# Kernel tuning notes

Hardware: AMD Instinct MI355X
Metric: run time of the kernel (lower is better)

The kernel has to match this reference:

```python
import jax, jax.numpy as jnp
import numpy as np


def setup_inputs() -> dict:
    key = jax.random.key(0)
    k1, k2, k3, k4 = jax.random.split(key, 4)
    B, L, H, E = 2, 10000, 8, 64
    NE = 160000
    return {
        "queries": jax.random.normal(k1, (B, L, H, E), dtype=jnp.float32),
        "keys": jax.random.normal(k2, (B, L, H, E), dtype=jnp.float32),
        "values": jax.random.normal(k3, (B, L, H, E), dtype=jnp.float32),
        "adj": jax.random.randint(k4, (2, NE), 0, L, dtype=jnp.int64),
    }


def reference(queries, keys, values, adj):
    # queries/keys/values: [B, L, H, E]; adj: [2, NE] (row 0 = dst group, row 1 = src)
    B, L, H, E = queries.shape
    softmax_temp = 1.0 / (E ** 0.5)
    dst = adj[0]
    src = adj[1]

    # edge-gather dot product: qk[b, e, h] = sum_d q[b, dst[e], h, d] * k[b, src[e], h, d]
    qk = jnp.sum(queries[:, dst] * keys[:, src], axis=-1) * softmax_temp  # [B, NE, H]

    # segment softmax grouped by destination node (dropout is identity at eval)
    qk_e = qk.transpose(1, 0, 2)  # [NE, B, H] (segment ops act on leading axis)
    seg_max = jax.ops.segment_max(qk_e, dst, num_segments=L)  # [L, B, H]
    ex = jnp.exp(qk_e - seg_max[dst])
    seg_sum = jax.ops.segment_sum(ex, dst, num_segments=L)  # [L, B, H]
    alpha = ex / (seg_sum[dst] + 1e-16)  # [NE, B, H]

    # spmm: gather v at src, weight by alpha, scatter-add to dst
    weighted = values[:, src] * alpha.transpose(1, 0, 2)[..., None]  # [B, NE, H, E]
    out = jnp.zeros_like(values).at[:, dst].add(weighted)  # [B, L, H, E]
    return out
```

## Files before the change

kernel.cpp:

```cpp
#include <hip/hip_runtime.h>

#define BB 2
#define HH 8
#define EE 64
#define ROW (HH * EE)
#define CHUNK 16

__device__ inline unsigned short f2bf(float f) {
  unsigned int u = __float_as_uint(f);
  u = (u + 0x7fffu + ((u >> 16) & 1u)) >> 16;
  return (unsigned short)u;
}

__global__ __launch_bounds__(256) void convert_kernel(
    const float* __restrict__ k, const float* __restrict__ v,
    unsigned short* __restrict__ kbf, unsigned short* __restrict__ vbf,
    int n4) {
  int i = blockIdx.x * blockDim.x + threadIdx.x;
  if (i >= n4) return;
  float4 kf = ((const float4*)k)[i];
  float4 vf = ((const float4*)v)[i];
  ushort4 ko = make_ushort4(f2bf(kf.x), f2bf(kf.y), f2bf(kf.z), f2bf(kf.w));
  ushort4 vo = make_ushort4(f2bf(vf.x), f2bf(vf.y), f2bf(vf.z), f2bf(vf.w));
  ((ushort4*)kbf)[i] = ko;
  ((ushort4*)vbf)[i] = vo;
}

__global__ __launch_bounds__(256) void hist_kernel(
    const int* __restrict__ dst, int* __restrict__ counts, int NE) {
  int e = blockIdx.x * blockDim.x + threadIdx.x;
  if (e >= NE) return;
  atomicAdd(&counts[dst[e]], 1);
}

__global__ __launch_bounds__(1024) void scan_kernel(
    const int* __restrict__ counts, int* __restrict__ offsets, int L) {
  __shared__ int sums[1024];
  int tid = threadIdx.x;
  int chunk = (L + 1023) / 1024;
  int beg = tid * chunk;
  int end = min(beg + chunk, L);
  int s = 0;
  for (int i = beg; i < end; ++i) s += counts[i];
  sums[tid] = s;
  __syncthreads();
  for (int off = 1; off < 1024; off <<= 1) {
    int val = 0;
    if (tid >= off) val = sums[tid - off];
    __syncthreads();
    if (tid >= off) sums[tid] += val;
    __syncthreads();
  }
  int run = (tid > 0) ? sums[tid - 1] : 0;
  for (int i = beg; i < end; ++i) {
    offsets[i] = run;
    run += counts[i];
  }
  if (tid == 1023) offsets[L] = run;
}

__global__ __launch_bounds__(256) void fill_csr_kernel(
    const int* __restrict__ dst, const int* __restrict__ src,
    const int* __restrict__ offsets, int* __restrict__ cursor,
    int* __restrict__ csr_src, int NE) {
  int e = blockIdx.x * blockDim.x + threadIdx.x;
  if (e >= NE) return;
  int d = dst[e];
  int pos = atomicAdd(&cursor[d], 1);
  csr_src[offsets[d] + pos] = src[e];
}

__device__ inline void bf8_unpack(uint4 u, float* f) {
  f[0] = __uint_as_float(u.x << 16);
  f[1] = __uint_as_float(u.x & 0xffff0000u);
  f[2] = __uint_as_float(u.y << 16);
  f[3] = __uint_as_float(u.y & 0xffff0000u);
  f[4] = __uint_as_float(u.z << 16);
  f[5] = __uint_as_float(u.z & 0xffff0000u);
  f[6] = __uint_as_float(u.w << 16);
  f[7] = __uint_as_float(u.w & 0xffff0000u);
}

__global__ __launch_bounds__(256) void fused_attn_kernel(
    const float* __restrict__ q, const unsigned short* __restrict__ kbf,
    const unsigned short* __restrict__ vbf, const int* __restrict__ offsets,
    const int* __restrict__ csr_src, float* __restrict__ out, int L) {
  int wid = blockIdx.x * (blockDim.x >> 6) + (threadIdx.x >> 6);
  int lane = threadIdx.x & 63;
  if (wid >= L * BB) return;
  int d = wid >> 1;
  int b = wid & 1;
  int beg = offsets[d];
  int end = offsets[d + 1];

  const float4* qrow = (const float4*)(q + ((size_t)b * L + d) * ROW);
  float4 q0 = qrow[lane * 2 + 0];
  float4 q1 = qrow[lane * 2 + 1];

  float m = -INFINITY;
  float l_run = 0.0f;
  float acc[8];
#pragma unroll
  for (int i = 0; i < 8; ++i) acc[i] = 0.0f;

  const uint4* kb_base = (const uint4*)(kbf + (size_t)b * L * ROW);
  const uint4* vb_base = (const uint4*)(vbf + (size_t)b * L * ROW);

  for (int t0 = beg; t0 < end; t0 += CHUNK) {
    int cnt = min(CHUNK, end - t0);
    float qk[CHUNK];
    int srcs[CHUNK];
    float cmax = -INFINITY;
#pragma unroll
    for (int i = 0; i < CHUNK; ++i) {
      qk[i] = -INFINITY;
      if (i < cnt) {
        int s = csr_src[t0 + i];
        srcs[i] = s;
        uint4 kk = kb_base[(size_t)s * (ROW / 8) + lane];
        float kf[8];
        bf8_unpack(kk, kf);
        float p = q0.x * kf[0] + q0.y * kf[1] + q0.z * kf[2] + q0.w * kf[3] +
                  q1.x * kf[4] + q1.y * kf[5] + q1.z * kf[6] + q1.w * kf[7];
        p += __shfl_xor(p, 1);
        p += __shfl_xor(p, 2);
        p += __shfl_xor(p, 4);
        p *= 0.125f;
        qk[i] = p;
        cmax = fmaxf(cmax, p);
      }
    }
    float mnew = fmaxf(m, cmax);
    float scale = __expf(m - mnew);
    l_run *= scale;
#pragma unroll
    for (int i = 0; i < 8; ++i) acc[i] *= scale;
    m = mnew;
#pragma unroll
    for (int i = 0; i < CHUNK; ++i) {
      if (i < cnt) {
        float a = __expf(qk[i] - m);
        l_run += a;
        uint4 vv = vb_base[(size_t)srcs[i] * (ROW / 8) + lane];
        float vf[8];
        bf8_unpack(vv, vf);
#pragma unroll
        for (int j = 0; j < 8; ++j) acc[j] += a * vf[j];
      }
    }
  }
  float r = 1.0f / (l_run + 1e-16f);
  float4* orow = (float4*)(out + ((size_t)b * L + d) * ROW);
  orow[lane * 2 + 0] = make_float4(acc[0] * r, acc[1] * r, acc[2] * r, acc[3] * r);
  orow[lane * 2 + 1] = make_float4(acc[4] * r, acc[5] * r, acc[6] * r, acc[7] * r);
}

extern "C" void kernel_launch(void* const* d_in, const int* in_sizes, int n_in,
                              void* d_out, int out_size, void* d_ws, size_t ws_size,
                              hipStream_t stream) {
  const float* q = (const float*)d_in[0];
  const float* k = (const float*)d_in[1];
  const float* v = (const float*)d_in[2];
  const int* adj = (const int*)d_in[3];

  const int NE = in_sizes[3] / 2;
  const int L = in_sizes[0] / (BB * HH * EE);
  const int* dst = adj;
  const int* src = adj + NE;
  const int nelem = BB * L * HH * EE;

  char* ws = (char*)d_ws;
  size_t off = 0;
  unsigned short* kbf = (unsigned short*)(ws + off); off += (size_t)nelem * 2;
  unsigned short* vbf = (unsigned short*)(ws + off); off += (size_t)nelem * 2;
  int* counts = (int*)(ws + off);   off += (size_t)L * 4;
  int* offsets = (int*)(ws + off);  off += (size_t)(L + 1) * 4;
  int* cursor = (int*)(ws + off);   off += (size_t)L * 4;
  int* csr_src = (int*)(ws + off);  off += (size_t)NE * 4;

  hipMemsetAsync(counts, 0, (size_t)L * 4, stream);
  hipMemsetAsync(cursor, 0, (size_t)L * 4, stream);

  int n4 = nelem / 4;
  convert_kernel<<<(n4 + 255) / 256, 256, 0, stream>>>(k, v, kbf, vbf, n4);

  hist_kernel<<<(NE + 255) / 256, 256, 0, stream>>>(dst, counts, NE);
  scan_kernel<<<1, 1024, 0, stream>>>(counts, offsets, L);
  fill_csr_kernel<<<(NE + 255) / 256, 256, 0, stream>>>(dst, src, offsets, cursor, csr_src, NE);

  int nwaves = L * BB;
  fused_attn_kernel<<<(nwaves + 3) / 4, 256, 0, stream>>>(
      q, kbf, vbf, offsets, csr_src, (float*)d_out, L);
}
```

Baseline: 287.8 us.

## Fuse convert with histogram, reuse counts as cursor, prefetch K/V per chunk

Folds the bf16 conversion and the destination histogram into one kernel. The scan now zeroes the counts array so fill_csr can reuse it as the cursor, which removes one memset, one buffer and one launch. In the attention kernel, all K and V rows for a chunk are loaded up front so the gather loads can be in flight together. CHUNK is halved to 8 to limit the extra register pressure from holding 16 uint4 values. The scan reads and writes counts through two __restrict__ pointers that alias the same array, but each thread reads an element before zeroing it, so it is likely safe.

```diff
diff --git a/kernel.cpp b/kernel.cpp
--- a/kernel.cpp
+++ b/kernel.cpp
@@ -4,7 +4,7 @@
 #define HH 8
 #define EE 64
 #define ROW (HH * EE)
-#define CHUNK 16
+#define CHUNK 8
 
 __device__ inline unsigned short f2bf(float f) {
   unsigned int u = __float_as_uint(f);
@@ -12,36 +12,33 @@
   return (unsigned short)u;
 }
 
-__global__ __launch_bounds__(256) void convert_kernel(
+__global__ __launch_bounds__(256) void convert_hist_kernel(
     const float* __restrict__ k, const float* __restrict__ v,
     unsigned short* __restrict__ kbf, unsigned short* __restrict__ vbf,
-    int n4) {
+    const int* __restrict__ dst, int* __restrict__ counts,
+    int n4, int NE) {
   int i = blockIdx.x * blockDim.x + threadIdx.x;
-  if (i >= n4) return;
-  float4 kf = ((const float4*)k)[i];
-  float4 vf = ((const float4*)v)[i];
-  ushort4 ko = make_ushort4(f2bf(kf.x), f2bf(kf.y), f2bf(kf.z), f2bf(kf.w));
-  ushort4 vo = make_ushort4(f2bf(vf.x), f2bf(vf.y), f2bf(vf.z), f2bf(vf.w));
-  ((ushort4*)kbf)[i] = ko;
-  ((ushort4*)vbf)[i] = vo;
-}
-
-__global__ __launch_bounds__(256) void hist_kernel(
-    const int* __restrict__ dst, int* __restrict__ counts, int NE) {
-  int e = blockIdx.x * blockDim.x + threadIdx.x;
-  if (e >= NE) return;
-  atomicAdd(&counts[dst[e]], 1);
+  if (i < n4) {
+    float4 kf = ((const float4*)k)[i];
+    float4 vf = ((const float4*)v)[i];
+    ((ushort4*)kbf)[i] = make_ushort4(f2bf(kf.x), f2bf(kf.y), f2bf(kf.z), f2bf(kf.w));
+    ((ushort4*)vbf)[i] = make_ushort4(f2bf(vf.x), f2bf(vf.y), f2bf(vf.z), f2bf(vf.w));
+  }
+  if (i < NE) {
+    atomicAdd(&counts[dst[i]], 1);
+  }
 }
 
 __global__ __launch_bounds__(1024) void scan_kernel(
-    const int* __restrict__ counts, int* __restrict__ offsets, int L) {
+    const int* __restrict__ counts_in, int* __restrict__ counts_mut,
+    int* __restrict__ offsets, int L) {
   __shared__ int sums[1024];
   int tid = threadIdx.x;
   int chunk = (L + 1023) / 1024;
   int beg = tid * chunk;
   int end = min(beg + chunk, L);
   int s = 0;
-  for (int i = beg; i < end; ++i) s += counts[i];
+  for (int i = beg; i < end; ++i) s += counts_in[i];
   sums[tid] = s;
   __syncthreads();
   for (int off = 1; off < 1024; off <<= 1) {
@@ -54,7 +51,8 @@
   int run = (tid > 0) ? sums[tid - 1] : 0;
   for (int i = beg; i < end; ++i) {
     offsets[i] = run;
-    run += counts[i];
+    run += counts_in[i];
+    counts_mut[i] = 0;
   }
   if (tid == 1023) offsets[L] = run;
 }
@@ -108,18 +106,23 @@
 
   for (int t0 = beg; t0 < end; t0 += CHUNK) {
     int cnt = min(CHUNK, end - t0);
+    uint4 kk[CHUNK], vv[CHUNK];
+#pragma unroll
+    for (int i = 0; i < CHUNK; ++i) {
+      if (i < cnt) {
+        int s = csr_src[t0 + i];
+        kk[i] = kb_base[(size_t)s * (ROW / 8) + lane];
+        vv[i] = vb_base[(size_t)s * (ROW / 8) + lane];
+      }
+    }
     float qk[CHUNK];
-    int srcs[CHUNK];
     float cmax = -INFINITY;
 #pragma unroll
     for (int i = 0; i < CHUNK; ++i) {
       qk[i] = -INFINITY;
       if (i < cnt) {
-        int s = csr_src[t0 + i];
-        srcs[i] = s;
-        uint4 kk = kb_base[(size_t)s * (ROW / 8) + lane];
         float kf[8];
-        bf8_unpack(kk, kf);
+        bf8_unpack(kk[i], kf);
         float p = q0.x * kf[0] + q0.y * kf[1] + q0.z * kf[2] + q0.w * kf[3] +
                   q1.x * kf[4] + q1.y * kf[5] + q1.z * kf[6] + q1.w * kf[7];
         p += __shfl_xor(p, 1);
@@ -141,9 +144,8 @@
       if (i < cnt) {
         float a = __expf(qk[i] - m);
         l_run += a;
-        uint4 vv = vb_base[(size_t)srcs[i] * (ROW / 8) + lane];
         float vf[8];
-        bf8_unpack(vv, vf);
+        bf8_unpack(vv[i], vf);
 #pragma unroll
         for (int j = 0; j < 8; ++j) acc[j] += a * vf[j];
       }
@@ -175,18 +177,18 @@
   unsigned short* vbf = (unsigned short*)(ws + off); off += (size_t)nelem * 2;
   int* counts = (int*)(ws + off);   off += (size_t)L * 4;
   int* offsets = (int*)(ws + off);  off += (size_t)(L + 1) * 4;
-  int* cursor = (int*)(ws + off);   off += (size_t)L * 4;
   int* csr_src = (int*)(ws + off);  off += (size_t)NE * 4;
 
   hipMemsetAsync(counts, 0, (size_t)L * 4, stream);
-  hipMemsetAsync(cursor, 0, (size_t)L * 4, stream);
 
   int n4 = nelem / 4;
-  convert_kernel<<<(n4 + 255) / 256, 256, 0, stream>>>(k, v, kbf, vbf, n4);
+  convert_hist_kernel<<<(n4 + 255) / 256, 256, 0, stream>>>(
+      k, v, kbf, vbf, dst, counts, n4, NE);
 
-  hist_kernel<<<(NE + 255) / 256, 256, 0, stream>>>(dst, counts, NE);
-  scan_kernel<<<1, 1024, 0, stream>>>(counts, offsets, L);
-  fill_csr_kernel<<<(NE + 255) / 256, 256, 0, stream>>>(dst, src, offsets, cursor, csr_src, NE);
+  scan_kernel<<<1, 1024, 0, stream>>>(counts, counts, offsets, L);
+
+  fill_csr_kernel<<<(NE + 255) / 256, 256, 0, stream>>>(
+      dst, src, offsets, counts, csr_src, NE);
 
   int nwaves = L * BB;
   fused_attn_kernel<<<(nwaves + 3) / 4, 256, 0, stream>>>(
```

New measurement: 283.7 us. About the same (-1.4%).
